# Performance work log

Hardware: AMD Instinct MI355X
Metric: run time of the kernel (lower is better)

Reference implementation:

```python
import jax, jax.numpy as jnp
import numpy as np

N_NODES = 100000
N_EDGES = 3200000
FEAT = 128
HID = 128
N_GRAPHS = 512


def setup_inputs() -> dict:
    key = jax.random.key(0)
    ks = jax.random.split(key, 16)
    x = jax.random.normal(ks[0], (N_NODES, FEAT), dtype=jnp.float32)
    edge_index = jax.random.randint(ks[1], (2, N_EDGES), 0, N_NODES, dtype=jnp.int32)
    edge_weight = jax.random.uniform(ks[2], (N_EDGES,), dtype=jnp.float32)
    batch = jnp.sort(jax.random.randint(ks[3], (N_NODES,), 0, N_GRAPHS, dtype=jnp.int32))
    s = 1.0 / np.sqrt(HID)
    W1 = jax.random.uniform(ks[4], (FEAT, HID), dtype=jnp.float32, minval=-s, maxval=s)
    W2 = jax.random.uniform(ks[5], (HID, HID), dtype=jnp.float32, minval=-s, maxval=s)
    W3 = jax.random.uniform(ks[6], (HID, HID), dtype=jnp.float32, minval=-s, maxval=s)
    W4 = jax.random.uniform(ks[7], (HID, HID), dtype=jnp.float32, minval=-s, maxval=s)
    b1 = jnp.zeros((HID,), jnp.float32)
    b2 = jnp.zeros((HID,), jnp.float32)
    b3 = jnp.zeros((HID,), jnp.float32)
    b4 = jnp.zeros((HID,), jnp.float32)
    Wc = jax.random.uniform(ks[8], (HID, 1), dtype=jnp.float32, minval=-s, maxval=s)
    bc = jnp.zeros((1,), jnp.float32)
    return dict(x=x, edge_index=edge_index, edge_weight=edge_weight, batch=batch,
                W1=W1, b1=b1, W2=W2, b2=b2, W3=W3, b3=b3, W4=W4, b4=b4, Wc=Wc, bc=bc)


def _gcn_norm(edge_index, edge_weight, n):
    # PyG gcn_norm with add_self_loops=True (self-loop weight 1)
    loop = jnp.arange(n, dtype=edge_index.dtype)
    src = jnp.concatenate([edge_index[0], loop])
    dst = jnp.concatenate([edge_index[1], loop])
    ew = jnp.concatenate([edge_weight, jnp.ones((n,), edge_weight.dtype)])
    deg = jax.ops.segment_sum(ew, dst, num_segments=n)
    dinv = jnp.where(deg > 0, jax.lax.rsqrt(jnp.maximum(deg, 1e-30)), 0.0)
    norm = dinv[src] * ew * dinv[dst]
    return src, dst, norm


def _gcn_conv(x, src, dst, norm, W, b, n):
    h = x @ W                      # [N, H] dense GEMM
    msg = h[src] * norm[:, None]   # [E+N, H] gather + scale
    out = jax.ops.segment_sum(msg, dst, num_segments=n)  # scatter-add
    return out + b


def reference(x, edge_index, edge_weight, batch,
              W1, b1, W2, b2, W3, b3, W4, b4, Wc, bc):
    n = x.shape[0]
    src, dst, norm = _gcn_norm(edge_index, edge_weight, n)
    h = jax.nn.relu(_gcn_conv(x, src, dst, norm, W1, b1, n))
    h = jax.nn.relu(_gcn_conv(h, src, dst, norm, W2, b2, n))
    h = jax.nn.relu(_gcn_conv(h, src, dst, norm, W3, b3, n))
    h = jax.nn.relu(_gcn_conv(h, src, dst, norm, W4, b4, n))
    # global mean pool over graphs
    sums = jax.ops.segment_sum(h, batch, num_segments=N_GRAPHS)
    cnt = jax.ops.segment_sum(jnp.ones((n,), h.dtype), batch, num_segments=N_GRAPHS)
    pooled = sums / jnp.maximum(cnt, 1.0)[:, None]
    return jax.nn.sigmoid(pooled @ Wc + bc)
```

## Files before the change

### kernel.cpp

```cpp
#include <hip/hip_runtime.h>
#include <math.h>


#define MASK40 ((1ull << 40) - 1)

typedef float v2f __attribute__((ext_vector_type(2)));
typedef __bf16 bf16x8 __attribute__((ext_vector_type(8)));
typedef float f32x4 __attribute__((ext_vector_type(4)));

__device__ inline unsigned f2bf(float x) {
    unsigned u = __float_as_uint(x);
    return (u + 0x7FFFu + ((u >> 16) & 1u)) >> 16;
}

__global__ void init_packed(unsigned long long* packed, int n) {
    int i = blockIdx.x * blockDim.x + threadIdx.x;
    if (i < n) packed[i] = 0ull;
}

__global__ void edge_pass(const int* __restrict__ dst, const float* __restrict__ ew,
                          unsigned long long* packed, unsigned short* __restrict__ slot,
                          int E) {
    int e = blockIdx.x * blockDim.x + threadIdx.x;
    if (e < E) {
        int d = dst[e];
        unsigned int fx = (unsigned int)rintf(ew[e] * 16777216.0f);
        unsigned long long old =
            atomicAdd(&packed[d], (1ull << 40) | (unsigned long long)fx);
        slot[e] = (unsigned short)(old >> 40);
    }
}

__global__ void dinv_cnt_k(const unsigned long long* __restrict__ packed,
                           float* dinv, int* cnt, int n) {
    int i = blockIdx.x * blockDim.x + threadIdx.x;
    if (i < n) {
        unsigned long long p = packed[i];
        float deg = 1.0f + (float)(p & MASK40) * (1.0f / 16777216.0f);
        dinv[i] = rsqrtf(deg);
        cnt[i] = (int)(p >> 40);
    }
}

__global__ __launch_bounds__(1024) void scan1(const int* __restrict__ cnt, int* rowp,
                                              int* bsums, int total, int N) {
    __shared__ int sh[1024];
    int i = blockIdx.x * 1024 + threadIdx.x;
    int v = 0;
    if (i < N) v = cnt[i] + 1;
    sh[threadIdx.x] = v;
    __syncthreads();
    for (int off = 1; off < 1024; off <<= 1) {
        int t = (threadIdx.x >= (unsigned)off) ? sh[threadIdx.x - off] : 0;
        __syncthreads();
        sh[threadIdx.x] += t;
        __syncthreads();
    }
    if (i < total) rowp[i] = sh[threadIdx.x] - v;
    if (threadIdx.x == 1023) bsums[blockIdx.x] = sh[1023];
}

__global__ void scan2(int* bsums, int nb) {
    if (threadIdx.x == 0 && blockIdx.x == 0) {
        int run = 0;
        for (int b = 0; b < nb; ++b) { int t = bsums[b]; bsums[b] = run; run += t; }
    }
}

__global__ __launch_bounds__(1024) void scan3(int* rowp, const int* __restrict__ bsums,
                                              int total) {
    int i = blockIdx.x * 1024 + threadIdx.x;
    if (i < total) rowp[i] += bsums[blockIdx.x];
}

__global__ void selfloop_k(const int* __restrict__ rowp, const float* __restrict__ dinv,
                           int2* colval, int n) {
    int i = blockIdx.x * blockDim.x + threadIdx.x;
    if (i < n) {
        float dv = dinv[i];
        int2 cv;
        cv.x = i;
        cv.y = __float_as_int(dv * dv);
        colval[rowp[i]] = cv;
    }
}

__global__ void scatter2(const int* __restrict__ src, const int* __restrict__ dst,
                         const float* __restrict__ ew,
                         const unsigned short* __restrict__ slot,
                         const float* __restrict__ dinv, const int* __restrict__ rowp,
                         int2* colval, int E) {
    int e = blockIdx.x * blockDim.x + threadIdx.x;
    if (e < E) {
        int s = src[e], d = dst[e];
        int idx = rowp[d] + 1 + (int)slot[e];
        int2 cv;
        cv.x = s;
        cv.y = __float_as_int(dinv[s] * ew[e] * dinv[d]);
        colval[idx] = cv;
    }
}

__global__ void cvt_x(const float2* __restrict__ x, unsigned* __restrict__ xb,
                      long n64) {
    long t = (long)blockIdx.x * 256 + threadIdx.x;
    if (t < n64) {
        float2 f = x[t];
        xb[t] = f2bf(f.x) | (f2bf(f.y) << 16);
    }
}

__global__ void prep_w(const float* __restrict__ Wa, const float* __restrict__ Wb,
                       const float* __restrict__ Wc, const float* __restrict__ Wd,
                       unsigned short* __restrict__ Wt) {
    const int l = blockIdx.y;
    const float* W = (l == 0) ? Wa : (l == 1) ? Wb : (l == 2) ? Wc : Wd;
    const int c = blockIdx.x, p = threadIdx.x;
    int k;
    if (l == 0) {
        k = p;
    } else {
        int t = p >> 1, h = p & 1;
        int i = t >> 2, s = (t >> 1) & 1, jj = 2 * (t & 1) + h;
        k = 16 * (4 * s + jj) + i;
    }
    float v = W[k * 128 + c];
    unsigned u = __float_as_uint(v);
    Wt[l * 16384 + c * 128 + p] = (unsigned short)((u + 0x7FFFu + ((u >> 16) & 1u)) >> 16);
}

__global__ __launch_bounds__(256) void gemm_mfma(const uint4* __restrict__ A,
                                                 const uint4* __restrict__ Wt,
                                                 uint2* __restrict__ C) {
    const int w = threadIdx.x >> 6;
    const int lane = threadIdx.x & 63;
    const int i = lane & 15, q = lane >> 4;
    const long row_base = (long)blockIdx.x * 64 + w * 16;

    f32x4 acc[8];
#pragma unroll
    for (int t = 0; t < 8; ++t) acc[t] = (f32x4){0.f, 0.f, 0.f, 0.f};

    const uint4* Arow = A + (row_base + i) * 16 + q;
#pragma unroll
    for (int ks = 0; ks < 4; ++ks) {
        const bf16x8 af = __builtin_bit_cast(bf16x8, Arow[ks * 4]);
#pragma unroll
        for (int ct = 0; ct < 8; ++ct) {
            const bf16x8 bf = __builtin_bit_cast(
                bf16x8, Wt[(size_t)(ct * 16 + i) * 16 + ks * 4 + q]);
            acc[ct] = __builtin_amdgcn_mfma_f32_16x16x32_bf16(af, bf, acc[ct], 0, 0, 0);
        }
    }

#pragma unroll
    for (int reg = 0; reg < 4; ++reg) {
        int d0 = __builtin_amdgcn_cvt_pk_fp8_f32(acc[0][reg], acc[1][reg], 0, false);
        d0     = __builtin_amdgcn_cvt_pk_fp8_f32(acc[2][reg], acc[3][reg], d0, true);
        int d1 = __builtin_amdgcn_cvt_pk_fp8_f32(acc[4][reg], acc[5][reg], 0, false);
        d1     = __builtin_amdgcn_cvt_pk_fp8_f32(acc[6][reg], acc[7][reg], d1, true);
        const long row = row_base + q * 4 + reg;
        uint2 o; o.x = (unsigned)d0; o.y = (unsigned)d1;
        C[row * 16 + i] = o;
    }
}

__device__ inline int perm_f0(int lane) {
    return 64 * ((lane >> 1) & 1) + 32 * (lane & 1) + (lane >> 2);
}

__global__ __launch_bounds__(64) void aggregate(const unsigned short* __restrict__ t8,
                                                const int* __restrict__ rowp,
                                                const int2* __restrict__ colval,
                                                const float* __restrict__ bias,
                                                unsigned* __restrict__ out16, int n) {
    const int v = blockIdx.x;
    const int lane = threadIdx.x;
    const int e0 = rowp[v], e1 = rowp[v + 1];
    float ax = 0.f, ay = 0.f;
    int e = e0;
    for (; e + 4 <= e1; e += 4) {
        const int2 cv0 = colval[e],     cv1 = colval[e + 1];
        const int2 cv2 = colval[e + 2], cv3 = colval[e + 3];
        const unsigned short u0 = t8[(size_t)cv0.x * 64 + lane];
        const unsigned short u1 = t8[(size_t)cv1.x * 64 + lane];
        const unsigned short u2 = t8[(size_t)cv2.x * 64 + lane];
        const unsigned short u3 = t8[(size_t)cv3.x * 64 + lane];
        const float w0 = __int_as_float(cv0.y), w1 = __int_as_float(cv1.y);
        const float w2 = __int_as_float(cv2.y), w3 = __int_as_float(cv3.y);
        const v2f h0 = __builtin_amdgcn_cvt_pk_f32_fp8((int)u0, false);
        const v2f h1 = __builtin_amdgcn_cvt_pk_f32_fp8((int)u1, false);
        const v2f h2 = __builtin_amdgcn_cvt_pk_f32_fp8((int)u2, false);
        const v2f h3 = __builtin_amdgcn_cvt_pk_f32_fp8((int)u3, false);
        ax = fmaf(w0, h0.x, ax); ay = fmaf(w0, h0.y, ay);
        ax = fmaf(w1, h1.x, ax); ay = fmaf(w1, h1.y, ay);
        ax = fmaf(w2, h2.x, ax); ay = fmaf(w2, h2.y, ay);
        ax = fmaf(w3, h3.x, ax); ay = fmaf(w3, h3.y, ay);
    }
    for (; e < e1; ++e) {
        const int2 cv = colval[e];
        const v2f hv = __builtin_amdgcn_cvt_pk_f32_fp8(
            (int)t8[(size_t)cv.x * 64 + lane], false);
        const float w = __int_as_float(cv.y);
        ax = fmaf(w, hv.x, ax); ay = fmaf(w, hv.y, ay);
    }
    const int f0 = perm_f0(lane);
    const float rx = fmaxf(ax + bias[f0], 0.f);
    const float ry = fmaxf(ay + bias[f0 + 16], 0.f);
    out16[(size_t)v * 64 + lane] = f2bf(rx) | (f2bf(ry) << 16);
}

__global__ __launch_bounds__(64) void aggregate_last(const unsigned short* __restrict__ t8,
                                                     const int* __restrict__ rowp,
                                                     const int2* __restrict__ colval,
                                                     const float* __restrict__ bias,
                                                     const float* __restrict__ Wc,
                                                     float* __restrict__ sv, int n) {
    const int v = blockIdx.x;
    const int lane = threadIdx.x;
    const int e0 = rowp[v], e1 = rowp[v + 1];
    float ax = 0.f, ay = 0.f;
    int e = e0;
    for (; e + 4 <= e1; e += 4) {
        const int2 cv0 = colval[e],     cv1 = colval[e + 1];
        const int2 cv2 = colval[e + 2], cv3 = colval[e + 3];
        const unsigned short u0 = t8[(size_t)cv0.x * 64 + lane];
        const unsigned short u1 = t8[(size_t)cv1.x * 64 + lane];
        const unsigned short u2 = t8[(size_t)cv2.x * 64 + lane];
        const unsigned short u3 = t8[(size_t)cv3.x * 64 + lane];
        const float w0 = __int_as_float(cv0.y), w1 = __int_as_float(cv1.y);
        const float w2 = __int_as_float(cv2.y), w3 = __int_as_float(cv3.y);
        const v2f h0 = __builtin_amdgcn_cvt_pk_f32_fp8((int)u0, false);
        const v2f h1 = __builtin_amdgcn_cvt_pk_f32_fp8((int)u1, false);
        const v2f h2 = __builtin_amdgcn_cvt_pk_f32_fp8((int)u2, false);
        const v2f h3 = __builtin_amdgcn_cvt_pk_f32_fp8((int)u3, false);
        ax = fmaf(w0, h0.x, ax); ay = fmaf(w0, h0.y, ay);
        ax = fmaf(w1, h1.x, ax); ay = fmaf(w1, h1.y, ay);
        ax = fmaf(w2, h2.x, ax); ay = fmaf(w2, h2.y, ay);
        ax = fmaf(w3, h3.x, ax); ay = fmaf(w3, h3.y, ay);
    }
    for (; e < e1; ++e) {
        const int2 cv = colval[e];
        const v2f hv = __builtin_amdgcn_cvt_pk_f32_fp8(
            (int)t8[(size_t)cv.x * 64 + lane], false);
        const float w = __int_as_float(cv.y);
        ax = fmaf(w, hv.x, ax); ay = fmaf(w, hv.y, ay);
    }
    const int f0 = perm_f0(lane);
    float p = fmaxf(ax + bias[f0], 0.f) * Wc[f0] +
              fmaxf(ay + bias[f0 + 16], 0.f) * Wc[f0 + 16];
#pragma unroll
    for (int off = 32; off; off >>= 1) p += __shfl_down(p, off);
    if (lane == 0) sv[v] = p;
}

__global__ void gstart_k(const int* __restrict__ batch, int* start, int N, int G) {
    int g = blockIdx.x * blockDim.x + threadIdx.x;
    if (g <= G) {
        int lo = 0, hi = N;
        while (lo < hi) {
            int mid = (lo + hi) >> 1;
            if (batch[mid] < g) lo = mid + 1; else hi = mid;
        }
        start[g] = lo;
    }
}

__global__ __launch_bounds__(256) void seg_pool(const float* __restrict__ sv,
                                                const int* __restrict__ start,
                                                const float* __restrict__ bc,
                                                float* __restrict__ out, int G) {
    __shared__ float sh[4];
    const int g = blockIdx.x;
    const int s = start[g], epos = start[g + 1];
    float acc = 0.f;
    for (int i = s + threadIdx.x; i < epos; i += 256) acc += sv[i];
#pragma unroll
    for (int off = 32; off; off >>= 1) acc += __shfl_down(acc, off);
    if ((threadIdx.x & 63) == 0) sh[threadIdx.x >> 6] = acc;
    __syncthreads();
    if (threadIdx.x == 0) {
        float sum = sh[0] + sh[1] + sh[2] + sh[3];
        float cnt = (float)(epos - s);
        float z = sum / fmaxf(cnt, 1.0f) + bc[0];
        out[g] = 1.0f / (1.0f + expf(-z));
    }
}

extern "C" void kernel_launch(void* const* d_in, const int* in_sizes, int n_in,
                              void* d_out, int out_size, void* d_ws, size_t ws_size,
                              hipStream_t stream) {
    const float* x   = (const float*)d_in[0];
    const int* ei    = (const int*)d_in[1];
    const float* ew  = (const float*)d_in[2];
    const int* batch = (const int*)d_in[3];
    const float* W1 = (const float*)d_in[4];  const float* b1 = (const float*)d_in[5];
    const float* W2 = (const float*)d_in[6];  const float* b2 = (const float*)d_in[7];
    const float* W3 = (const float*)d_in[8];  const float* b3 = (const float*)d_in[9];
    const float* W4 = (const float*)d_in[10]; const float* b4 = (const float*)d_in[11];
    const float* Wc = (const float*)d_in[12]; const float* bc = (const float*)d_in[13];

    const int N = in_sizes[0] / 128;
    const int E = in_sizes[2];
    const int G = out_size;
    const int* src = ei;
    const int* dst = ei + E;
    const int nblk = (N + 63) / 64;
    const long Npad = (long)nblk * 64;

    char* p = (char*)d_ws;
    auto alloc = [&](size_t bytes) {
        void* q = (void*)p;
        p += (bytes + 255) & ~(size_t)255;
        return q;
    };
    unsigned long long* packed = (unsigned long long*)alloc((size_t)N * 8);
    float* dinv = (float*)alloc((size_t)N * 4);
    int* cnt    = (int*)alloc((size_t)N * 4);
    unsigned short* slot = (unsigned short*)alloc((size_t)E * 2);
    int* rowp   = (int*)alloc((size_t)(N + 1) * 4);
    int* bsums  = (int*)alloc(1024 * 4);
    const size_t M = (size_t)E + (size_t)N;
    int2* colval = (int2*)alloc(M * 8);
    unsigned* tbuf = (unsigned*)alloc((size_t)Npad * 32 * 4);
    unsigned* hbuf = (unsigned*)alloc((size_t)Npad * 64 * 4);
    unsigned* xb   = (unsigned*)alloc((size_t)Npad * 64 * 4);
    unsigned short* Wt = (unsigned short*)alloc(4 * 16384 * 2);
    float* sv   = (float*)alloc((size_t)N * 4);
    int* start  = (int*)alloc((size_t)(G + 1) * 4);

    const int B = 256;
    init_packed<<<(N + B - 1) / B, B, 0, stream>>>(packed, N);
    edge_pass<<<(E + B - 1) / B, B, 0, stream>>>(dst, ew, packed, slot, E);
    dinv_cnt_k<<<(N + B - 1) / B, B, 0, stream>>>(packed, dinv, cnt, N);
    const int total = N + 1;
    const int nb = (total + 1023) / 1024;
    scan1<<<nb, 1024, 0, stream>>>(cnt, rowp, bsums, total, N);
    scan2<<<1, 64, 0, stream>>>(bsums, nb);
    scan3<<<nb, 1024, 0, stream>>>(rowp, bsums, total);
    selfloop_k<<<(N + B - 1) / B, B, 0, stream>>>(rowp, dinv, colval, N);
    scatter2<<<(E + B - 1) / B, B, 0, stream>>>(src, dst, ew, slot, dinv, rowp,
                                                colval, E);
    gstart_k<<<(G + 1 + B - 1) / B, B, 0, stream>>>(batch, start, N, G);

    const long n64 = (long)N * 64;
    cvt_x<<<(int)((n64 + 255) / 256), B, 0, stream>>>((const float2*)x, xb, n64);
    prep_w<<<dim3(128, 4), 128, 0, stream>>>(W1, W2, W3, W4, Wt);

    const unsigned short* t8 = (const unsigned short*)tbuf;
    const uint4* Wt4 = (const uint4*)Wt;
    gemm_mfma<<<nblk, B, 0, stream>>>((const uint4*)xb,   Wt4,         (uint2*)tbuf);
    aggregate<<<N, 64, 0, stream>>>(t8, rowp, colval, b1, hbuf, N);
    gemm_mfma<<<nblk, B, 0, stream>>>((const uint4*)hbuf, Wt4 + 2048,  (uint2*)tbuf);
    aggregate<<<N, 64, 0, stream>>>(t8, rowp, colval, b2, hbuf, N);
    gemm_mfma<<<nblk, B, 0, stream>>>((const uint4*)hbuf, Wt4 + 4096,  (uint2*)tbuf);
    aggregate<<<N, 64, 0, stream>>>(t8, rowp, colval, b3, hbuf, N);
    gemm_mfma<<<nblk, B, 0, stream>>>((const uint4*)hbuf, Wt4 + 6144,  (uint2*)tbuf);
    aggregate_last<<<N, 64, 0, stream>>>(t8, rowp, colval, b4, Wc, sv, N);

    seg_pool<<<G, B, 0, stream>>>(sv, start, bc, (float*)d_out, G);
}
```

Baseline: 859.9 us.

## Fuse x conversion into GEMM, merge degree into scan, two-node aggregate blocks

The separate fp32-to-bf16 conversion of x is folded into the first GEMM through a template flag, which removes one full pass over x and its staging buffer. The dinv/count kernel is merged into scan1, and the init kernel is replaced by hipMemsetAsync. The aggregation kernels now handle two nodes per 64-lane block, with each half-wave gathering 4 bytes (four fp8 features) per lane instead of 2. This halves the block count and widens loads, at the cost of divergence when the two nodes have unequal degree: the shorter node makes redundant clamped loads with zero weight.

```diff
diff --git a/kernel.cpp b/kernel.cpp
--- a/kernel.cpp
+++ b/kernel.cpp
@@ -11,11 +11,6 @@
 __device__ inline unsigned f2bf(float x) {
     unsigned u = __float_as_uint(x);
     return (u + 0x7FFFu + ((u >> 16) & 1u)) >> 16;
-}
-
-__global__ void init_packed(unsigned long long* packed, int n) {
-    int i = blockIdx.x * blockDim.x + threadIdx.x;
-    if (i < n) packed[i] = 0ull;
 }
 
 __global__ void edge_pass(const int* __restrict__ dst, const float* __restrict__ ew,
@@ -31,23 +26,18 @@
     }
 }
 
-__global__ void dinv_cnt_k(const unsigned long long* __restrict__ packed,
-                           float* dinv, int* cnt, int n) {
-    int i = blockIdx.x * blockDim.x + threadIdx.x;
-    if (i < n) {
-        unsigned long long p = packed[i];
-        float deg = 1.0f + (float)(p & MASK40) * (1.0f / 16777216.0f);
-        dinv[i] = rsqrtf(deg);
-        cnt[i] = (int)(p >> 40);
-    }
-}
-
-__global__ __launch_bounds__(1024) void scan1(const int* __restrict__ cnt, int* rowp,
+__global__ __launch_bounds__(1024) void scan1(const unsigned long long* __restrict__ packed,
+                                              float* __restrict__ dinv, int* rowp,
                                               int* bsums, int total, int N) {
     __shared__ int sh[1024];
     int i = blockIdx.x * 1024 + threadIdx.x;
     int v = 0;
-    if (i < N) v = cnt[i] + 1;
+    if (i < N) {
+        unsigned long long p = packed[i];
+        float deg = 1.0f + (float)(p & MASK40) * (1.0f / 16777216.0f);
+        dinv[i] = rsqrtf(deg);
+        v = (int)(p >> 40) + 1;
+    }
     sh[threadIdx.x] = v;
     __syncthreads();
     for (int off = 1; off < 1024; off <<= 1) {
@@ -101,15 +91,6 @@
     }
 }
 
-__global__ void cvt_x(const float2* __restrict__ x, unsigned* __restrict__ xb,
-                      long n64) {
-    long t = (long)blockIdx.x * 256 + threadIdx.x;
-    if (t < n64) {
-        float2 f = x[t];
-        xb[t] = f2bf(f.x) | (f2bf(f.y) << 16);
-    }
-}
-
 __global__ void prep_w(const float* __restrict__ Wa, const float* __restrict__ Wb,
                        const float* __restrict__ Wc, const float* __restrict__ Wd,
                        unsigned short* __restrict__ Wt) {
@@ -129,26 +110,41 @@
     Wt[l * 16384 + c * 128 + p] = (unsigned short)((u + 0x7FFFu + ((u >> 16) & 1u)) >> 16);
 }
 
-__global__ __launch_bounds__(256) void gemm_mfma(const uint4* __restrict__ A,
+template <int FP32IN>
+__global__ __launch_bounds__(256) void gemm_mfma(const void* __restrict__ Av,
                                                  const uint4* __restrict__ Wt,
-                                                 uint2* __restrict__ C) {
+                                                 uint2* __restrict__ C, int N) {
     const int w = threadIdx.x >> 6;
     const int lane = threadIdx.x & 63;
-    const int i = lane & 15, q = lane >> 4;
+    const int li = lane & 15, q = lane >> 4;
     const long row_base = (long)blockIdx.x * 64 + w * 16;
+    const long arow = (row_base + li < (long)N) ? row_base + li : (long)N - 1;
 
     f32x4 acc[8];
 #pragma unroll
     for (int t = 0; t < 8; ++t) acc[t] = (f32x4){0.f, 0.f, 0.f, 0.f};
 
-    const uint4* Arow = A + (row_base + i) * 16 + q;
 #pragma unroll
     for (int ks = 0; ks < 4; ++ks) {
-        const bf16x8 af = __builtin_bit_cast(bf16x8, Arow[ks * 4]);
+        bf16x8 af;
+        if (FP32IN) {
+            const float* Ar = (const float*)Av + arow * 128 + ks * 32 + q * 8;
+            const float4 fa = *(const float4*)Ar;
+            const float4 fb = *(const float4*)(Ar + 4);
+            uint4 u;
+            u.x = f2bf(fa.x) | (f2bf(fa.y) << 16);
+            u.y = f2bf(fa.z) | (f2bf(fa.w) << 16);
+            u.z = f2bf(fb.x) | (f2bf(fb.y) << 16);
+            u.w = f2bf(fb.z) | (f2bf(fb.w) << 16);
+            af = __builtin_bit_cast(bf16x8, u);
+        } else {
+            af = __builtin_bit_cast(bf16x8,
+                ((const uint4*)Av)[arow * 16 + ks * 4 + q]);
+        }
 #pragma unroll
         for (int ct = 0; ct < 8; ++ct) {
             const bf16x8 bf = __builtin_bit_cast(
-                bf16x8, Wt[(size_t)(ct * 16 + i) * 16 + ks * 4 + q]);
+                bf16x8, Wt[(size_t)(ct * 16 + li) * 16 + ks * 4 + q]);
             acc[ct] = __builtin_amdgcn_mfma_f32_16x16x32_bf16(af, bf, acc[ct], 0, 0, 0);
         }
     }
@@ -161,97 +157,140 @@
         d1     = __builtin_amdgcn_cvt_pk_fp8_f32(acc[6][reg], acc[7][reg], d1, true);
         const long row = row_base + q * 4 + reg;
         uint2 o; o.x = (unsigned)d0; o.y = (unsigned)d1;
-        C[row * 16 + i] = o;
-    }
-}
-
-__device__ inline int perm_f0(int lane) {
-    return 64 * ((lane >> 1) & 1) + 32 * (lane & 1) + (lane >> 2);
-}
-
-__global__ __launch_bounds__(64) void aggregate(const unsigned short* __restrict__ t8,
-                                                const int* __restrict__ rowp,
-                                                const int2* __restrict__ colval,
-                                                const float* __restrict__ bias,
-                                                unsigned* __restrict__ out16, int n) {
-    const int v = blockIdx.x;
+        C[row * 16 + li] = o;
+    }
+}
+
+__global__ __launch_bounds__(64) void aggregate2(const unsigned* __restrict__ t32,
+                                                 const int* __restrict__ rowp,
+                                                 const int2* __restrict__ colval,
+                                                 const float* __restrict__ bias,
+                                                 unsigned* __restrict__ out16, int n) {
+    const int v0 = blockIdx.x * 2;
     const int lane = threadIdx.x;
-    const int e0 = rowp[v], e1 = rowp[v + 1];
-    float ax = 0.f, ay = 0.f;
-    int e = e0;
-    for (; e + 4 <= e1; e += 4) {
-        const int2 cv0 = colval[e],     cv1 = colval[e + 1];
-        const int2 cv2 = colval[e + 2], cv3 = colval[e + 3];
-        const unsigned short u0 = t8[(size_t)cv0.x * 64 + lane];
-        const unsigned short u1 = t8[(size_t)cv1.x * 64 + lane];
-        const unsigned short u2 = t8[(size_t)cv2.x * 64 + lane];
-        const unsigned short u3 = t8[(size_t)cv3.x * 64 + lane];
-        const float w0 = __int_as_float(cv0.y), w1 = __int_as_float(cv1.y);
-        const float w2 = __int_as_float(cv2.y), w3 = __int_as_float(cv3.y);
-        const v2f h0 = __builtin_amdgcn_cvt_pk_f32_fp8((int)u0, false);
-        const v2f h1 = __builtin_amdgcn_cvt_pk_f32_fp8((int)u1, false);
-        const v2f h2 = __builtin_amdgcn_cvt_pk_f32_fp8((int)u2, false);
-        const v2f h3 = __builtin_amdgcn_cvt_pk_f32_fp8((int)u3, false);
-        ax = fmaf(w0, h0.x, ax); ay = fmaf(w0, h0.y, ay);
-        ax = fmaf(w1, h1.x, ax); ay = fmaf(w1, h1.y, ay);
-        ax = fmaf(w2, h2.x, ax); ay = fmaf(w2, h2.y, ay);
-        ax = fmaf(w3, h3.x, ax); ay = fmaf(w3, h3.y, ay);
-    }
-    for (; e < e1; ++e) {
-        const int2 cv = colval[e];
-        const v2f hv = __builtin_amdgcn_cvt_pk_f32_fp8(
-            (int)t8[(size_t)cv.x * 64 + lane], false);
-        const float w = __int_as_float(cv.y);
-        ax = fmaf(w, hv.x, ax); ay = fmaf(w, hv.y, ay);
-    }
-    const int f0 = perm_f0(lane);
-    const float rx = fmaxf(ax + bias[f0], 0.f);
-    const float ry = fmaxf(ay + bias[f0 + 16], 0.f);
-    out16[(size_t)v * 64 + lane] = f2bf(rx) | (f2bf(ry) << 16);
-}
-
-__global__ __launch_bounds__(64) void aggregate_last(const unsigned short* __restrict__ t8,
-                                                     const int* __restrict__ rowp,
-                                                     const int2* __restrict__ colval,
-                                                     const float* __restrict__ bias,
-                                                     const float* __restrict__ Wc,
-                                                     float* __restrict__ sv, int n) {
-    const int v = blockIdx.x;
+    const int h = lane >> 5, il = lane & 31;
+
+    const int base0 = rowp[v0];
+    const int mid   = rowp[v0 + 1];
+    const bool have1 = (v0 + 1) < n;
+    const int end1  = have1 ? rowp[v0 + 2] : mid;
+    const int len0 = mid - base0;
+    const int len1 = end1 - mid;
+    const int maxlen = (len0 > len1) ? len0 : len1;
+    const int lenh = h ? len1 : len0;
+
+    float a0 = 0.f, a1 = 0.f, a2 = 0.f, a3 = 0.f;
+    int j = 0;
+    for (; j + 4 <= maxlen; j += 4) {
+#pragma unroll
+        for (int k = 0; k < 4; ++k) {
+            const int jj = j + k;
+            const int j0 = (jj < len0) ? jj : len0 - 1;
+            const int j1 = (jj < len1) ? jj : len1 - 1;
+            const int2 ca = colval[base0 + j0];
+            const int2 cb = colval[mid + j1];
+            const int c = h ? cb.x : ca.x;
+            float w = __int_as_float(h ? cb.y : ca.y);
+            w = (jj < lenh) ? w : 0.f;
+            const unsigned u = t32[(size_t)c * 32 + il];
+            const v2f lo = __builtin_amdgcn_cvt_pk_f32_fp8((int)u, false);
+            const v2f hi = __builtin_amdgcn_cvt_pk_f32_fp8((int)u, true);
+            a0 = fmaf(w, lo.x, a0); a1 = fmaf(w, lo.y, a1);
+            a2 = fmaf(w, hi.x, a2); a3 = fmaf(w, hi.y, a3);
+        }
+    }
+    for (; j < maxlen; ++j) {
+        const int j0 = (j < len0) ? j : len0 - 1;
+        const int j1 = (j < len1) ? j : len1 - 1;
+        const int2 ca = colval[base0 + j0];
+        const int2 cb = colval[mid + j1];
+        const int c = h ? cb.x : ca.x;
+        float w = __int_as_float(h ? cb.y : ca.y);
+        w = (j < lenh) ? w : 0.f;
+        const unsigned u = t32[(size_t)c * 32 + il];
+        const v2f lo = __builtin_amdgcn_cvt_pk_f32_fp8((int)u, false);
+        const v2f hi = __builtin_amdgcn_cvt_pk_f32_fp8((int)u, true);
+        a0 = fmaf(w, lo.x, a0); a1 = fmaf(w, lo.y, a1);
+        a2 = fmaf(w, hi.x, a2); a3 = fmaf(w, hi.y, a3);
+    }
+
+    const int f0 = 64 * (il & 1) + (il >> 1);
+    const float r0 = fmaxf(a0 + bias[f0],      0.f);
+    const float r1 = fmaxf(a1 + bias[f0 + 16], 0.f);
+    const float r2 = fmaxf(a2 + bias[f0 + 32], 0.f);
+    const float r3 = fmaxf(a3 + bias[f0 + 48], 0.f);
+    const int v = v0 + h;
+    if (v < n) {
+        uint2 o;
+        o.x = f2bf(r0) | (f2bf(r1) << 16);
+        o.y = f2bf(r2) | (f2bf(r3) << 16);
+        *(uint2*)&out16[(size_t)v * 64 + il * 2] = o;
+    }
+}
+
+__global__ __launch_bounds__(64) void aggregate2_last(const unsigned* __restrict__ t32,
+                                                      const int* __restrict__ rowp,
+                                                      const int2* __restrict__ colval,
+                                                      const float* __restrict__ bias,
+                                                      const float* __restrict__ Wc,
+                                                      float* __restrict__ sv, int n) {
+    const int v0 = blockIdx.x * 2;
     const int lane = threadIdx.x;
-    const int e0 = rowp[v], e1 = rowp[v + 1];
-    float ax = 0.f, ay = 0.f;
-    int e = e0;
-    for (; e + 4 <= e1; e += 4) {
-        const int2 cv0 = colval[e],     cv1 = colval[e + 1];
-        const int2 cv2 = colval[e + 2], cv3 = colval[e + 3];
-        const unsigned short u0 = t8[(size_t)cv0.x * 64 + lane];
-        const unsigned short u1 = t8[(size_t)cv1.x * 64 + lane];
-        const unsigned short u2 = t8[(size_t)cv2.x * 64 + lane];
-        const unsigned short u3 = t8[(size_t)cv3.x * 64 + lane];
-        const float w0 = __int_as_float(cv0.y), w1 = __int_as_float(cv1.y);
-        const float w2 = __int_as_float(cv2.y), w3 = __int_as_float(cv3.y);
-        const v2f h0 = __builtin_amdgcn_cvt_pk_f32_fp8((int)u0, false);
-        const v2f h1 = __builtin_amdgcn_cvt_pk_f32_fp8((int)u1, false);
-        const v2f h2 = __builtin_amdgcn_cvt_pk_f32_fp8((int)u2, false);
-        const v2f h3 = __builtin_amdgcn_cvt_pk_f32_fp8((int)u3, false);
-        ax = fmaf(w0, h0.x, ax); ay = fmaf(w0, h0.y, ay);
-        ax = fmaf(w1, h1.x, ax); ay = fmaf(w1, h1.y, ay);
-        ax = fmaf(w2, h2.x, ax); ay = fmaf(w2, h2.y, ay);
-        ax = fmaf(w3, h3.x, ax); ay = fmaf(w3, h3.y, ay);
-    }
-    for (; e < e1; ++e) {
-        const int2 cv = colval[e];
-        const v2f hv = __builtin_amdgcn_cvt_pk_f32_fp8(
-            (int)t8[(size_t)cv.x * 64 + lane], false);
-        const float w = __int_as_float(cv.y);
-        ax = fmaf(w, hv.x, ax); ay = fmaf(w, hv.y, ay);
-    }
-    const int f0 = perm_f0(lane);
-    float p = fmaxf(ax + bias[f0], 0.f) * Wc[f0] +
-              fmaxf(ay + bias[f0 + 16], 0.f) * Wc[f0 + 16];
-#pragma unroll
-    for (int off = 32; off; off >>= 1) p += __shfl_down(p, off);
-    if (lane == 0) sv[v] = p;
+    const int h = lane >> 5, il = lane & 31;
+
+    const int base0 = rowp[v0];
+    const int mid   = rowp[v0 + 1];
+    const bool have1 = (v0 + 1) < n;
+    const int end1  = have1 ? rowp[v0 + 2] : mid;
+    const int len0 = mid - base0;
+    const int len1 = end1 - mid;
+    const int maxlen = (len0 > len1) ? len0 : len1;
+    const int lenh = h ? len1 : len0;
+
+    float a0 = 0.f, a1 = 0.f, a2 = 0.f, a3 = 0.f;
+    int j = 0;
+    for (; j + 4 <= maxlen; j += 4) {
+#pragma unroll
+        for (int k = 0; k < 4; ++k) {
+            const int jj = j + k;
+            const int j0 = (jj < len0) ? jj : len0 - 1;
+            const int j1 = (jj < len1) ? jj : len1 - 1;
+            const int2 ca = colval[base0 + j0];
+            const int2 cb = colval[mid + j1];
+            const int c = h ? cb.x : ca.x;
+            float w = __int_as_float(h ? cb.y : ca.y);
+            w = (jj < lenh) ? w : 0.f;
+            const unsigned u = t32[(size_t)c * 32 + il];
+            const v2f lo = __builtin_amdgcn_cvt_pk_f32_fp8((int)u, false);
+            const v2f hi = __builtin_amdgcn_cvt_pk_f32_fp8((int)u, true);
+            a0 = fmaf(w, lo.x, a0); a1 = fmaf(w, lo.y, a1);
+            a2 = fmaf(w, hi.x, a2); a3 = fmaf(w, hi.y, a3);
+        }
+    }
+    for (; j < maxlen; ++j) {
+        const int j0 = (j < len0) ? j : len0 - 1;
+        const int j1 = (j < len1) ? j : len1 - 1;
+        const int2 ca = colval[base0 + j0];
+        const int2 cb = colval[mid + j1];
+        const int c = h ? cb.x : ca.x;
+        float w = __int_as_float(h ? cb.y : ca.y);
+        w = (j < lenh) ? w : 0.f;
+        const unsigned u = t32[(size_t)c * 32 + il];
+        const v2f lo = __builtin_amdgcn_cvt_pk_f32_fp8((int)u, false);
+        const v2f hi = __builtin_amdgcn_cvt_pk_f32_fp8((int)u, true);
+        a0 = fmaf(w, lo.x, a0); a1 = fmaf(w, lo.y, a1);
+        a2 = fmaf(w, hi.x, a2); a3 = fmaf(w, hi.y, a3);
+    }
+
+    const int f0 = 64 * (il & 1) + (il >> 1);
+    float p = fmaxf(a0 + bias[f0],      0.f) * Wc[f0]
+            + fmaxf(a1 + bias[f0 + 16], 0.f) * Wc[f0 + 16]
+            + fmaxf(a2 + bias[f0 + 32], 0.f) * Wc[f0 + 32]
+            + fmaxf(a3 + bias[f0 + 48], 0.f) * Wc[f0 + 48];
+#pragma unroll
+    for (int off = 16; off; off >>= 1) p += __shfl_xor(p, off);
+    const int v = v0 + h;
+    if (il == 0 && v < n) sv[v] = p;
 }
 
 __global__ void gstart_k(const int* __restrict__ batch, int* start, int N, int G) {
@@ -316,7 +355,6 @@
     };
     unsigned long long* packed = (unsigned long long*)alloc((size_t)N * 8);
     float* dinv = (float*)alloc((size_t)N * 4);
-    int* cnt    = (int*)alloc((size_t)N * 4);
     unsigned short* slot = (unsigned short*)alloc((size_t)E * 2);
     int* rowp   = (int*)alloc((size_t)(N + 1) * 4);
     int* bsums  = (int*)alloc(1024 * 4);
@@ -324,39 +362,34 @@
     int2* colval = (int2*)alloc(M * 8);
     unsigned* tbuf = (unsigned*)alloc((size_t)Npad * 32 * 4);
     unsigned* hbuf = (unsigned*)alloc((size_t)Npad * 64 * 4);
-    unsigned* xb   = (unsigned*)alloc((size_t)Npad * 64 * 4);
     unsigned short* Wt = (unsigned short*)alloc(4 * 16384 * 2);
     float* sv   = (float*)alloc((size_t)N * 4);
     int* start  = (int*)alloc((size_t)(G + 1) * 4);
 
     const int B = 256;
-    init_packed<<<(N + B - 1) / B, B, 0, stream>>>(packed, N);
+    hipMemsetAsync(packed, 0, (size_t)N * 8, stream);
     edge_pass<<<(E + B - 1) / B, B, 0, stream>>>(dst, ew, packed, slot, E);
-    dinv_cnt_k<<<(N + B - 1) / B, B, 0, stream>>>(packed, dinv, cnt, N);
     const int total = N + 1;
     const int nb = (total + 1023) / 1024;
-    scan1<<<nb, 1024, 0, stream>>>(cnt, rowp, bsums, total, N);
+    scan1<<<nb, 1024, 0, stream>>>(packed, dinv, rowp, bsums, total, N);
     scan2<<<1, 64, 0, stream>>>(bsums, nb);
     scan3<<<nb, 1024, 0, stream>>>(rowp, bsums, total);
     selfloop_k<<<(N + B - 1) / B, B, 0, stream>>>(rowp, dinv, colval, N);
     scatter2<<<(E + B - 1) / B, B, 0, stream>>>(src, dst, ew, slot, dinv, rowp,
                                                 colval, E);
     gstart_k<<<(G + 1 + B - 1) / B, B, 0, stream>>>(batch, start, N, G);
-
-    const long n64 = (long)N * 64;
-    cvt_x<<<(int)((n64 + 255) / 256), B, 0, stream>>>((const float2*)x, xb, n64);
     prep_w<<<dim3(128, 4), 128, 0, stream>>>(W1, W2, W3, W4, Wt);
 
-    const unsigned short* t8 = (const unsigned short*)tbuf;
+    const int agrid = (N + 1) / 2;
     const uint4* Wt4 = (const uint4*)Wt;
-    gemm_mfma<<<nblk, B, 0, stream>>>((const uint4*)xb,   Wt4,         (uint2*)tbuf);
-    aggregate<<<N, 64, 0, stream>>>(t8, rowp, colval, b1, hbuf, N);
-    gemm_mfma<<<nblk, B, 0, stream>>>((const uint4*)hbuf, Wt4 + 2048,  (uint2*)tbuf);
-    aggregate<<<N, 64, 0, stream>>>(t8, rowp, colval, b2, hbuf, N);
-    gemm_mfma<<<nblk, B, 0, stream>>>((const uint4*)hbuf, Wt4 + 4096,  (uint2*)tbuf);
-    aggregate<<<N, 64, 0, stream>>>(t8, rowp, colval, b3, hbuf, N);
-    gemm_mfma<<<nblk, B, 0, stream>>>((const uint4*)hbuf, Wt4 + 6144,  (uint2*)tbuf);
-    aggregate_last<<<N, 64, 0, stream>>>(t8, rowp, colval, b4, Wc, sv, N);
+    gemm_mfma<1><<<nblk, B, 0, stream>>>(x,    Wt4,        (uint2*)tbuf, N);
+    aggregate2<<<agrid, 64, 0, stream>>>(tbuf, rowp, colval, b1, hbuf, N);
+    gemm_mfma<0><<<nblk, B, 0, stream>>>(hbuf, Wt4 + 2048, (uint2*)tbuf, N);
+    aggregate2<<<agrid, 64, 0, stream>>>(tbuf, rowp, colval, b2, hbuf, N);
+    gemm_mfma<0><<<nblk, B, 0, stream>>>(hbuf, Wt4 + 4096, (uint2*)tbuf, N);
+    aggregate2<<<agrid, 64, 0, stream>>>(tbuf, rowp, colval, b3, hbuf, N);
+    gemm_mfma<0><<<nblk, B, 0, stream>>>(hbuf, Wt4 + 6144, (uint2*)tbuf, N);
+    aggregate2_last<<<agrid, 64, 0, stream>>>(tbuf, rowp, colval, b4, Wc, sv, N);
 
     seg_pool<<<G, B, 0, stream>>>(sv, start, bc, (float*)d_out, G);
 }
```

After: 816.7 us. 1.05x faster.
